# Performance work log

Hardware: AMD Instinct MI355X
Metric: run time of the kernel (lower is better)

Reference implementation:

```python
import jax, jax.numpy as jnp
import numpy as np
import math

B, S, E, H = 4, 2048, 1024, 16
D = E // H  # head_dim = 64
ROPE_BASE = 10000.0


def setup_inputs() -> dict:
    key = jax.random.key(0)
    ks = jax.random.split(key, 8)
    wscale = 1.0 / math.sqrt(E)
    inp = {
        "query": jax.random.normal(ks[0], (B, S, E), dtype=jnp.float32),
        "key": jax.random.normal(ks[1], (B, S, E), dtype=jnp.float32),
        "value": jax.random.normal(ks[2], (B, S, E), dtype=jnp.float32),
        "Wq": jax.random.normal(ks[3], (E, E), dtype=jnp.float32) * wscale,
        "Wk": jax.random.normal(ks[4], (E, E), dtype=jnp.float32) * wscale,
        "Wv": jax.random.normal(ks[5], (E, E), dtype=jnp.float32) * wscale,
        "Wo": jax.random.normal(ks[6], (E, E), dtype=jnp.float32) * wscale,
        "positions": jnp.arange(S, dtype=jnp.int64),
        # True = masked (upper triangle -> causal)
        "attn_mask": jnp.triu(jnp.ones((S, S), dtype=bool), k=1),
    }
    return inp


def _apply_rope(x, positions):
    # x: [B, H, S, D]; rotate-half RoPE convention
    half = D // 2
    inv_freq = 1.0 / (ROPE_BASE ** (jnp.arange(0, D, 2, dtype=jnp.float32) / D))  # [D/2]
    ang = positions.astype(jnp.float32)[:, None] * inv_freq[None, :]  # [S, D/2]
    cos = jnp.concatenate([jnp.cos(ang), jnp.cos(ang)], axis=-1)  # [S, D]
    sin = jnp.concatenate([jnp.sin(ang), jnp.sin(ang)], axis=-1)  # [S, D]
    x1, x2 = x[..., :half], x[..., half:]
    rot = jnp.concatenate([-x2, x1], axis=-1)
    return x * cos[None, None] + rot * sin[None, None]


def reference(query, key, value, Wq, Wk, Wv, Wo, positions, attn_mask):
    # projections (no bias, weight layout [out, in] as in set_weights_from_float)
    q = jnp.einsum('bse,oe->bso', query, Wq).reshape(B, S, H, D).transpose(0, 2, 1, 3)
    k = jnp.einsum('bse,oe->bso', key, Wk).reshape(B, S, H, D).transpose(0, 2, 1, 3)
    v = jnp.einsum('bse,oe->bso', value, Wv).reshape(B, S, H, D).transpose(0, 2, 1, 3)
    q = _apply_rope(q, positions)
    k = _apply_rope(k, positions)
    scale = 1.0 / math.sqrt(D)
    scores = jnp.einsum('bhqd,bhkd->bhqk', q, k) * scale  # [B,H,S,S]
    scores = jnp.where(attn_mask[None, None], -jnp.inf, scores)
    weights = jax.nn.softmax(scores, axis=-1)
    out = jnp.einsum('bhqk,bhkd->bhqd', weights, v)  # [B,H,S,D]
    out = out.transpose(0, 2, 1, 3).reshape(B, S, H * D)
    return jnp.einsum('bso,eo->bse', out, Wo)
```

## Files before the change

### kernel.cpp

```cpp
#include <hip/hip_runtime.h>
#include <hip/hip_bf16.h>
#include <math.h>

typedef __bf16 bf16;
typedef __attribute__((ext_vector_type(8))) __bf16 bf16x8;
typedef __attribute__((ext_vector_type(4))) __bf16 bf16x4;
typedef __attribute__((ext_vector_type(4))) float f32x4;
typedef __attribute__((ext_vector_type(16))) float f32x16;
typedef __attribute__((ext_vector_type(4))) unsigned uint4v;

#define MFMA16 __builtin_amdgcn_mfma_f32_16x16x32_bf16
#define MFMA32 __builtin_amdgcn_mfma_f32_32x32x16_bf16

__device__ __forceinline__ void g2l16(const void* g, void* l) {
    __builtin_amdgcn_global_load_lds(
        (const __attribute__((address_space(1))) void*)g,
        (__attribute__((address_space(3))) void*)l, 16, 0, 0);
}

__device__ __forceinline__ bool is_bf16_buf(const void* p) {
    const int lane = threadIdx.x & 63;
    unsigned w = ((const unsigned*)p)[lane];
    unsigned e = (w >> 7) & 0xFF;
    bool pl = (e == 0) || (e >= 80 && e < 134);
    return __popcll(__ballot(pl)) >= 52;
}

__device__ __forceinline__ void stage_f32(bf16* l, const float* g) {
    float4 f0 = ((const float4*)g)[0];
    float4 f1 = ((const float4*)g)[1];
    bf16x8 t;
    t[0] = (bf16)f0.x; t[1] = (bf16)f0.y; t[2] = (bf16)f0.z; t[3] = (bf16)f0.w;
    t[4] = (bf16)f1.x; t[5] = (bf16)f1.y; t[6] = (bf16)f1.z; t[7] = (bf16)f1.w;
    *(bf16x8*)l = t;
}

__device__ __forceinline__ unsigned cvtpk_bf16(float a, float b) {
    unsigned r;
    asm("v_cvt_pk_bf16_f32 %0, %1, %2" : "=v"(r) : "v"(a), "v"(b));
    return r;
}

__global__ __launch_bounds__(256) void convert7(const void* s0, const void* s1,
                                                const void* s2, const void* s3,
                                                const void* s4, const void* s5,
                                                const void* s6,
                                                bf16* __restrict__ dst) {
    const size_t e = ((size_t)blockIdx.x * 256 + threadIdx.x) * 8;
    const void* src; size_t off; bf16* d;
    if (e < 25165824) {
        const int i = (int)(e >> 23);
        src = i == 0 ? s0 : i == 1 ? s1 : s2;
        off = e & 8388607;
        d   = dst + ((size_t)i << 23) + off;
    } else {
        const size_t e2 = e - 25165824;
        const int i = (int)(e2 >> 20);
        src = i == 0 ? s3 : i == 1 ? s4 : i == 2 ? s5 : s6;
        off = e2 & 1048575;
        d   = dst + 25165824 + ((size_t)i << 20) + off;
    }
    if (is_bf16_buf(src)) {
        *(bf16x8*)d = *((const bf16x8*)((const bf16*)src + off));
    } else {
        stage_f32(d, (const float*)src + off);
    }
}

__device__ __forceinline__ void epi_rope(f32x4 acc[4][4], bf16* __restrict__ C,
                                         int m0, int n0, int wm, int wn,
                                         int quad, int l16, float scale) {
    const float kf = 0.41524101186092029f;
    const float inv0 = exp2f(-(float)l16 * kf);
    const float inv1 = exp2f(-(float)(l16 + 16) * kf);
#pragma unroll
    for (int mi = 0; mi < 4; mi++) {
#pragma unroll
        for (int r = 0; r < 4; r++) {
            const int row = m0 + wm + mi * 16 + quad * 4 + r;
            const float pos = (float)(row & 2047);
#pragma unroll
            for (int p = 0; p < 2; p++) {
                float sn, cs;
                __sincosf(pos * (p ? inv1 : inv0), &sn, &cs);
                const float x1 = acc[mi][p][r];
                const float x2 = acc[mi][p + 2][r];
                const int col = n0 + wn + p * 16 + l16;
                C[(size_t)row * 1024 + col]      = (bf16)((x1 * cs - x2 * sn) * scale);
                C[(size_t)row * 1024 + col + 32] = (bf16)((x2 * cs + x1 * sn) * scale);
            }
        }
    }
}

__device__ __forceinline__ void epi_vt(f32x4 acc[4][4], bf16* __restrict__ C,
                                       int m0, int n0, int wm, int wn,
                                       int quad, int l16) {
#pragma unroll
    for (int mi = 0; mi < 4; mi++) {
        const int rbase = m0 + wm + mi * 16 + quad * 4;
#pragma unroll
        for (int ni = 0; ni < 4; ni++) {
            const int col = n0 + wn + ni * 16 + l16;
            bf16x4 t;
#pragma unroll
            for (int r = 0; r < 4; r++) t[r] = (bf16)acc[mi][ni][r];
            *(bf16x4*)&C[(size_t)col * 8192 + rbase] = t;
        }
    }
}

__global__ __launch_bounds__(256) void gemm_qkv(const bf16* __restrict__ xq,
                                                const bf16* __restrict__ xk,
                                                const bf16* __restrict__ xv,
                                                const bf16* __restrict__ wq,
                                                const bf16* __restrict__ wk,
                                                const bf16* __restrict__ wv,
                                                bf16* __restrict__ Qp,
                                                bf16* __restrict__ Kp,
                                                bf16* __restrict__ Vt) {
    __shared__ bf16 As[128 * 32];
    __shared__ bf16 Bs[128 * 32];
    const int tid  = threadIdx.x;
    const int wave = tid >> 6;
    const int lane = tid & 63;
    const int quad = lane >> 4;
    const int l16  = lane & 15;
    const int z  = blockIdx.z;
    const int m0 = blockIdx.x * 128;
    const int n0 = blockIdx.y * 128;
    const int wm = (wave >> 1) * 64;
    const int wn = (wave & 1) * 64;

    const bf16* A = z == 0 ? xq : z == 1 ? xk : xv;
    const bf16* W = z == 0 ? wq : z == 1 ? wk : wv;

    const int ra = tid >> 2;
    const int c8 = (tid & 3) * 8;
    const bf16* ga = A + (size_t)(m0 + ra) * 1024 + c8;
    const bf16* gb = W + (size_t)(n0 + ra) * 1024 + c8;
    bf16* lA0 = As + (wave * 64) * 8;
    bf16* lA1 = As + (256 + wave * 64) * 8;
    bf16* lB0 = Bs + (wave * 64) * 8;
    bf16* lB1 = Bs + (256 + wave * 64) * 8;

    f32x4 acc[4][4] = {};

    for (int k0 = 0; k0 < 1024; k0 += 32) {
        __syncthreads();
        g2l16(ga + k0,             lA0);
        g2l16(ga + 64 * 1024 + k0, lA1);
        g2l16(gb + k0,             lB0);
        g2l16(gb + 64 * 1024 + k0, lB1);
        __syncthreads();

        bf16x8 af[4], bfb[4];
#pragma unroll
        for (int i = 0; i < 4; i++)
            af[i] = *(const bf16x8*)&As[(wm + i * 16 + l16) * 32 + quad * 8];
#pragma unroll
        for (int i = 0; i < 4; i++)
            bfb[i] = *(const bf16x8*)&Bs[(wn + i * 16 + l16) * 32 + quad * 8];
#pragma unroll
        for (int mi = 0; mi < 4; mi++)
#pragma unroll
            for (int ni = 0; ni < 4; ni++)
                acc[mi][ni] = MFMA16(af[mi], bfb[ni], acc[mi][ni], 0, 0, 0);
    }

    if (z == 0)      epi_rope(acc, Qp, m0, n0, wm, wn, quad, l16, 0.125f);
    else if (z == 1) epi_rope(acc, Kp, m0, n0, wm, wn, quad, l16, 1.0f);
    else             epi_vt  (acc, Vt, m0, n0, wm, wn, quad, l16);
}

__global__ __launch_bounds__(256) void gemm_nt(const void* __restrict__ Ap,
                                               const void* __restrict__ Wp,
                                               bf16* __restrict__ C,
                                               float* __restrict__ Cf,
                                               int mode, float scale) {
    __shared__ bf16 As[128 * 32];
    __shared__ bf16 Bs[128 * 32];
    const int tid  = threadIdx.x;
    const int wave = tid >> 6;
    const int lane = tid & 63;
    const int quad = lane >> 4;
    const int l16  = lane & 15;
    const int m0 = blockIdx.x * 128;
    const int n0 = blockIdx.y * 128;
    const int wm = (wave >> 1) * 64;
    const int wn = (wave & 1) * 64;

    const bool a_bf = is_bf16_buf(Ap);
    const bool b_bf = is_bf16_buf(Wp);

    const int ra = tid >> 2;
    const int c8 = (tid & 3) * 8;
    const bf16*  gaB = (const bf16*)Ap  + (size_t)(m0 + ra) * 1024 + c8;
    const bf16*  gbB = (const bf16*)Wp  + (size_t)(n0 + ra) * 1024 + c8;
    const float* gaF = (const float*)Ap + (size_t)(m0 + ra) * 1024 + c8;
    const float* gbF = (const float*)Wp + (size_t)(n0 + ra) * 1024 + c8;
    bf16* lA0 = As + (wave * 64) * 8;
    bf16* lA1 = As + (256 + wave * 64) * 8;
    bf16* lB0 = Bs + (wave * 64) * 8;
    bf16* lB1 = Bs + (256 + wave * 64) * 8;

    f32x4 acc[4][4] = {};

    for (int k0 = 0; k0 < 1024; k0 += 32) {
        __syncthreads();
        if (a_bf) {
            g2l16(gaB + k0,             lA0);
            g2l16(gaB + 64 * 1024 + k0, lA1);
        } else {
            stage_f32(As + tid * 8,        gaF + k0);
            stage_f32(As + 2048 + tid * 8, gaF + 64 * 1024 + k0);
        }
        if (b_bf) {
            g2l16(gbB + k0,             lB0);
            g2l16(gbB + 64 * 1024 + k0, lB1);
        } else {
            stage_f32(Bs + tid * 8,        gbF + k0);
            stage_f32(Bs + 2048 + tid * 8, gbF + 64 * 1024 + k0);
        }
        __syncthreads();

        bf16x8 af[4], bfb[4];
#pragma unroll
        for (int i = 0; i < 4; i++)
            af[i] = *(const bf16x8*)&As[(wm + i * 16 + l16) * 32 + quad * 8];
#pragma unroll
        for (int i = 0; i < 4; i++)
            bfb[i] = *(const bf16x8*)&Bs[(wn + i * 16 + l16) * 32 + quad * 8];
#pragma unroll
        for (int mi = 0; mi < 4; mi++)
#pragma unroll
            for (int ni = 0; ni < 4; ni++)
                acc[mi][ni] = MFMA16(af[mi], bfb[ni], acc[mi][ni], 0, 0, 0);
    }

    if (mode == 2) {
#pragma unroll
        for (int mi = 0; mi < 4; mi++) {
            const int rbase = m0 + wm + mi * 16 + quad * 4;
#pragma unroll
            for (int ni = 0; ni < 4; ni++) {
                const int col = n0 + wn + ni * 16 + l16;
#pragma unroll
                for (int r = 0; r < 4; r++)
                    Cf[(size_t)(rbase + r) * 1024 + col] = acc[mi][ni][r];
            }
        }
    } else if (mode == 3) {
        epi_vt(acc, C, m0, n0, wm, wn, quad, l16);
    } else if (mode == 0) {
#pragma unroll
        for (int mi = 0; mi < 4; mi++) {
            const int rbase = m0 + wm + mi * 16 + quad * 4;
#pragma unroll
            for (int ni = 0; ni < 4; ni++) {
                const int col = n0 + wn + ni * 16 + l16;
#pragma unroll
                for (int r = 0; r < 4; r++)
                    C[(size_t)(rbase + r) * 1024 + col] = (bf16)acc[mi][ni][r];
            }
        }
    } else {
        epi_rope(acc, C, m0, n0, wm, wn, quad, l16, scale);
    }
}

__global__ __launch_bounds__(512, 2) void attn_kernel(const bf16* __restrict__ Qp,
                                                      const bf16* __restrict__ Kp,
                                                      const bf16* __restrict__ Vt,
                                                      bf16* __restrict__ Op) {
    __shared__ bf16 Ks[2][64 * 64];
    __shared__ bf16 Vs[2][64 * 64];
    __shared__ bf16 Qs[256 * 64];
    const int tid  = threadIdx.x;
    const int wave = tid >> 6;
    const int lane = tid & 63;
    const int l31  = lane & 31;
    const int hi   = lane >> 5;
    const int bh = blockIdx.x;
    const int y  = blockIdx.y;
    const int qt = (y < 4) ? y : 11 - y;
    const int b  = bh >> 4;
    const int h  = bh & 15;
    const int q0 = qt * 256;
    const int jmax = 4 * qt + 3;
    const size_t baseqk = ((size_t)b * 2048) * 1024 + (size_t)h * 64;
    const bf16* Qg = Qp + baseqk;
    const bf16* Kg = Kp + baseqk;
    const bf16* Vg = Vt + (size_t)(h * 64) * 8192 + (size_t)b * 2048;
    bf16* Og = Op + baseqk;

    const int sr  = tid >> 3;
    const int swz = (((tid & 7) ^ (sr & 7)) * 8);

#pragma unroll
    for (int c = 0; c < 4; c++)
        g2l16(Qg + (size_t)(q0 + c * 64 + sr) * 1024 + swz, Qs + c * 4096 + wave * 512);
    g2l16(Kg + (size_t)sr * 1024 + swz, &Ks[0][wave * 512]);
    g2l16(Vg + (size_t)sr * 8192 + swz, &Vs[0][wave * 512]);
    __syncthreads();

    const int qr = wave * 32 + l31;
    bf16x8 qf[4];
#pragma unroll
    for (int t = 0; t < 4; t++)
        qf[t] = *(const bf16x8*)&Qs[qr * 64 + (((2 * t + hi) ^ (l31 & 7)) * 8)];

    bf16x8 ones;
#pragma unroll
    for (int i = 0; i < 8; i++) ones[i] = (bf16)1.0f;

    f32x16 o0 = {}, o1 = {}, lacc = {};

    for (int j = 0; j <= jmax; j++) {
        if (j) __syncthreads();
        if (j < jmax) {
            const int pb = (j + 1) & 1;
            g2l16(Kg + (size_t)((j + 1) * 64 + sr) * 1024 + swz, &Ks[pb][wave * 512]);
            g2l16(Vg + (size_t)sr * 8192 + (j + 1) * 64 + swz,   &Vs[pb][wave * 512]);
        }
        if (q0 + wave * 32 + 31 < j * 64) continue;
        const bf16* kb = Ks[j & 1];
        const bf16* vb = Vs[j & 1];

        f32x16 s0 = {}, s1 = {};
        __builtin_amdgcn_s_setprio(1);
#pragma unroll
        for (int t = 0; t < 4; t++) {
            const int g = ((2 * t + hi) ^ (l31 & 7)) * 8;
            bf16x8 kf0 = *(const bf16x8*)&kb[l31 * 64 + g];
            bf16x8 kf1 = *(const bf16x8*)&kb[(32 + l31) * 64 + g];
            s0 = MFMA32(kf0, qf[t], s0, 0, 0, 0);
            s1 = MFMA32(kf1, qf[t], s1, 0, 0, 0);
        }
        __builtin_amdgcn_s_setprio(0);

        if (j * 64 + 63 > q0 + wave * 32) {
            const int qg  = q0 + wave * 32 + l31;
            const int kb0 = j * 64 + 4 * hi;
#pragma unroll
            for (int r = 0; r < 16; r++) {
                const int krow = (r & 3) + 8 * (r >> 2);
                if (kb0 + krow > qg)      s0[r] = -INFINITY;
                if (kb0 + 32 + krow > qg) s1[r] = -INFINITY;
            }
        }

#pragma unroll
        for (int r = 0; r < 16; r++) {
            s0[r] = __expf(s0[r] - 12.0f);
            s1[r] = __expf(s1[r] - 12.0f);
        }

        __builtin_amdgcn_s_setprio(1);
#pragma unroll
        for (int ks = 0; ks < 4; ks++) {
            const f32x16 p = (ks < 2) ? s0 : s1;
            const int rb = 8 * (ks & 1);
            unsigned x0 = cvtpk_bf16(p[rb + 0], p[rb + 1]);
            unsigned x1 = cvtpk_bf16(p[rb + 2], p[rb + 3]);
            unsigned y0 = cvtpk_bf16(p[rb + 4], p[rb + 5]);
            unsigned y1 = cvtpk_bf16(p[rb + 6], p[rb + 7]);
            auto r0 = __builtin_amdgcn_permlane32_swap(x0, y0, false, false);
            auto r1 = __builtin_amdgcn_permlane32_swap(x1, y1, false, false);
            uint4v pw;
            pw.x = (unsigned)r0[0];
            pw.y = (unsigned)r1[0];
            pw.z = (unsigned)r0[1];
            pw.w = (unsigned)r1[1];
            const bf16x8 pa = __builtin_bit_cast(bf16x8, pw);

            lacc = MFMA32(pa, ones, lacc, 0, 0, 0);
            const int g = ((2 * ks + hi) ^ (l31 & 7)) * 8;
            bf16x8 vf0 = *(const bf16x8*)&vb[l31 * 64 + g];
            bf16x8 vf1 = *(const bf16x8*)&vb[(32 + l31) * 64 + g];
            o0 = MFMA32(pa, vf0, o0, 0, 0, 0);
            o1 = MFMA32(pa, vf1, o1, 0, 0, 0);
        }
        __builtin_amdgcn_s_setprio(0);
    }

#pragma unroll
    for (int r = 0; r < 16; r++) {
        const float linv = 1.0f / lacc[r];
        const int row = q0 + wave * 32 + (r & 3) + 8 * (r >> 2) + 4 * hi;
        Og[(size_t)row * 1024 + l31]      = (bf16)(o0[r] * linv);
        Og[(size_t)row * 1024 + 32 + l31] = (bf16)(o1[r] * linv);
    }
}

extern "C" void kernel_launch(void* const* d_in, const int* in_sizes, int n_in,
                              void* d_out, int out_size, void* d_ws, size_t ws_size,
                              hipStream_t stream) {
    const void* q  = d_in[0];
    const void* k  = d_in[1];
    const void* v  = d_in[2];
    const void* Wq = d_in[3];
    const void* Wk = d_in[4];
    const void* Wv = d_in[5];
    const void* Wo = d_in[6];
    float* out = (float*)d_out;

    const size_t M8 = (size_t)8192 * 1024;
    bf16* Qp  = (bf16*)d_ws;
    bf16* Kp  = Qp + M8;
    bf16* Vtp = Kp + M8;
    bf16* Ao  = Vtp + M8;
    bf16* cbase = Ao + M8;
    const size_t NEED = (M8 * 4 + 29360128) * sizeof(bf16);

    dim3 blk(256);
    dim3 gg(64, 8);

    if (ws_size >= NEED) {
        convert7<<<14336, blk, 0, stream>>>(q, k, v, Wq, Wk, Wv, Wo, cbase);
        const bf16* aq = cbase;
        const bf16* ak = cbase + M8;
        const bf16* av = cbase + 2 * M8;
        const bf16* wq = cbase + 3 * M8;
        const bf16* wk = wq + 1048576;
        const bf16* wv = wk + 1048576;
        const bf16* wo = wv + 1048576;
        gemm_qkv<<<dim3(64, 8, 3), blk, 0, stream>>>(aq, ak, av, wq, wk, wv,
                                                     Qp, Kp, Vtp);
        attn_kernel<<<dim3(64, 8), dim3(512), 0, stream>>>(Qp, Kp, Vtp, Ao);
        gemm_nt<<<gg, blk, 0, stream>>>(Ao, wo, nullptr, out, 2, 1.0f);
    } else {
        gemm_nt<<<gg, blk, 0, stream>>>(q, Wq, Qp, nullptr, 1, 0.125f);
        gemm_nt<<<gg, blk, 0, stream>>>(k, Wk, Kp, nullptr, 1, 1.0f);
        gemm_nt<<<gg, blk, 0, stream>>>(v, Wv, Vtp, nullptr, 3, 1.0f);
        attn_kernel<<<dim3(64, 8), dim3(512), 0, stream>>>(Qp, Kp, Vtp, Ao);
        gemm_nt<<<gg, blk, 0, stream>>>(Ao, Wo, nullptr, out, 2, 1.0f);
    }
}
```

Before: 307.5 us.

## Replace projection GEMMs with triple-buffered swizzled 128x256 MFMA core

Adds a shared GEMM core that uses 512-thread blocks with 128x256 tiles, a K-step of 64, and a three-stage LDS ring filled by direct global-to-LDS loads. Explicit vmcnt waits let loads for later tiles overlap with MFMA work, and an XOR swizzle on the LDS layout is meant to avoid bank conflicts. Both the QKV projection and the output projection use this core, replacing the old single-buffered 128x128 kernel that synchronised twice per 32-wide K step. The larger tiles halve the grid and use more LDS per block, which may lower occupancy.

```diff
diff --git a/kernel.cpp b/kernel.cpp
--- a/kernel.cpp
+++ b/kernel.cpp
@@ -110,67 +110,127 @@
     }
 }
 
-__global__ __launch_bounds__(256) void gemm_qkv(const bf16* __restrict__ xq,
-                                                const bf16* __restrict__ xk,
-                                                const bf16* __restrict__ xv,
-                                                const bf16* __restrict__ wq,
-                                                const bf16* __restrict__ wk,
-                                                const bf16* __restrict__ wv,
-                                                bf16* __restrict__ Qp,
-                                                bf16* __restrict__ Kp,
-                                                bf16* __restrict__ Vt) {
-    __shared__ bf16 As[128 * 32];
-    __shared__ bf16 Bs[128 * 32];
+__device__ __forceinline__ void gemm_core(const bf16* __restrict__ A,
+                                          const bf16* __restrict__ B,
+                                          int m0, int n0, f32x4 acc[4][4]) {
+    __shared__ bf16 As[3 * 8192];
+    __shared__ bf16 Bs[3 * 16384];
     const int tid  = threadIdx.x;
     const int wave = tid >> 6;
     const int lane = tid & 63;
     const int quad = lane >> 4;
     const int l16  = lane & 15;
+    const int wm   = (wave >> 2) * 64;
+    const int wn   = (wave & 3) * 64;
+    const int rowt = tid >> 3;
+    const int swz  = (((tid & 7) ^ (rowt & 7)) * 8);
+    const bf16* gA = A + (size_t)(m0 + rowt) * 1024 + swz;
+    const bf16* gB = B + (size_t)(n0 + rowt) * 1024 + swz;
+    bf16* AsW = As + wave * 512;
+    bf16* BsW = Bs + wave * 512;
+
+#define STAGE(t, b)                                                     \
+    do {                                                                \
+        const int k0_ = (t) * 64;                                       \
+        g2l16(gA + k0_,          AsW + (b) * 8192);                     \
+        g2l16(gA + 65536 + k0_,  AsW + (b) * 8192 + 4096);              \
+        g2l16(gB + k0_,          BsW + (b) * 16384);                    \
+        g2l16(gB + 65536 + k0_,  BsW + (b) * 16384 + 4096);             \
+        g2l16(gB + 131072 + k0_, BsW + (b) * 16384 + 8192);             \
+        g2l16(gB + 196608 + k0_, BsW + (b) * 16384 + 12288);            \
+    } while (0)
+
+    STAGE(0, 0);
+    STAGE(1, 1);
+
+    const int gsw0 = ((0 + quad) ^ (l16 & 7)) * 8;
+    const int gsw1 = ((4 + quad) ^ (l16 & 7)) * 8;
+
+#pragma unroll
+    for (int t = 0; t < 16; t++) {
+        if (t < 15) asm volatile("s_waitcnt vmcnt(6)" ::: "memory");
+        else        asm volatile("s_waitcnt vmcnt(0)" ::: "memory");
+        __builtin_amdgcn_s_barrier();
+        __builtin_amdgcn_sched_barrier(0);
+        if (t <= 13) STAGE(t + 2, (t + 2) % 3);
+        __builtin_amdgcn_sched_barrier(0);
+        const bf16* At = As + (t % 3) * 8192;
+        const bf16* Bt = Bs + (t % 3) * 16384;
+#pragma unroll
+        for (int kk = 0; kk < 2; kk++) {
+            const int gg = kk ? gsw1 : gsw0;
+            bf16x8 af[4], bfr[4];
+#pragma unroll
+            for (int i = 0; i < 4; i++)
+                af[i] = *(const bf16x8*)&At[(wm + i * 16 + l16) * 64 + gg];
+#pragma unroll
+            for (int i = 0; i < 4; i++)
+                bfr[i] = *(const bf16x8*)&Bt[(wn + i * 16 + l16) * 64 + gg];
+            __builtin_amdgcn_s_setprio(1);
+#pragma unroll
+            for (int mi = 0; mi < 4; mi++)
+#pragma unroll
+                for (int ni = 0; ni < 4; ni++)
+                    acc[mi][ni] = MFMA16(af[mi], bfr[ni], acc[mi][ni], 0, 0, 0);
+            __builtin_amdgcn_s_setprio(0);
+            __builtin_amdgcn_sched_barrier(0);
+            if (kk == 0) __builtin_amdgcn_s_barrier();
+        }
+    }
+#undef STAGE
+}
+
+__global__ __launch_bounds__(512) void qkv256(const bf16* __restrict__ xq,
+                                              const bf16* __restrict__ xk,
+                                              const bf16* __restrict__ xv,
+                                              const bf16* __restrict__ wq,
+                                              const bf16* __restrict__ wk,
+                                              const bf16* __restrict__ wv,
+                                              bf16* __restrict__ Qp,
+                                              bf16* __restrict__ Kp,
+                                              bf16* __restrict__ Vt) {
     const int z  = blockIdx.z;
     const int m0 = blockIdx.x * 128;
-    const int n0 = blockIdx.y * 128;
-    const int wm = (wave >> 1) * 64;
-    const int wn = (wave & 1) * 64;
-
+    const int n0 = blockIdx.y * 256;
     const bf16* A = z == 0 ? xq : z == 1 ? xk : xv;
     const bf16* W = z == 0 ? wq : z == 1 ? wk : wv;
-
-    const int ra = tid >> 2;
-    const int c8 = (tid & 3) * 8;
-    const bf16* ga = A + (size_t)(m0 + ra) * 1024 + c8;
-    const bf16* gb = W + (size_t)(n0 + ra) * 1024 + c8;
-    bf16* lA0 = As + (wave * 64) * 8;
-    bf16* lA1 = As + (256 + wave * 64) * 8;
-    bf16* lB0 = Bs + (wave * 64) * 8;
-    bf16* lB1 = Bs + (256 + wave * 64) * 8;
-
     f32x4 acc[4][4] = {};
-
-    for (int k0 = 0; k0 < 1024; k0 += 32) {
-        __syncthreads();
-        g2l16(ga + k0,             lA0);
-        g2l16(ga + 64 * 1024 + k0, lA1);
-        g2l16(gb + k0,             lB0);
-        g2l16(gb + 64 * 1024 + k0, lB1);
-        __syncthreads();
-
-        bf16x8 af[4], bfb[4];
-#pragma unroll
-        for (int i = 0; i < 4; i++)
-            af[i] = *(const bf16x8*)&As[(wm + i * 16 + l16) * 32 + quad * 8];
-#pragma unroll
-        for (int i = 0; i < 4; i++)
-            bfb[i] = *(const bf16x8*)&Bs[(wn + i * 16 + l16) * 32 + quad * 8];
-#pragma unroll
-        for (int mi = 0; mi < 4; mi++)
-#pragma unroll
-            for (int ni = 0; ni < 4; ni++)
-                acc[mi][ni] = MFMA16(af[mi], bfb[ni], acc[mi][ni], 0, 0, 0);
-    }
-
+    gemm_core(A, W, m0, n0, acc);
+    const int wave = threadIdx.x >> 6;
+    const int lane = threadIdx.x & 63;
+    const int quad = lane >> 4;
+    const int l16  = lane & 15;
+    const int wm = (wave >> 2) * 64;
+    const int wn = (wave & 3) * 64;
     if (z == 0)      epi_rope(acc, Qp, m0, n0, wm, wn, quad, l16, 0.125f);
     else if (z == 1) epi_rope(acc, Kp, m0, n0, wm, wn, quad, l16, 1.0f);
     else             epi_vt  (acc, Vt, m0, n0, wm, wn, quad, l16);
+}
+
+__global__ __launch_bounds__(512) void out256(const bf16* __restrict__ Ao,
+                                              const bf16* __restrict__ wo,
+                                              float* __restrict__ Cf) {
+    const int m0 = blockIdx.x * 128;
+    const int n0 = blockIdx.y * 256;
+    f32x4 acc[4][4] = {};
+    gemm_core(Ao, wo, m0, n0, acc);
+    const int wave = threadIdx.x >> 6;
+    const int lane = threadIdx.x & 63;
+    const int quad = lane >> 4;
+    const int l16  = lane & 15;
+    const int wm = (wave >> 2) * 64;
+    const int wn = (wave & 3) * 64;
+#pragma unroll
+    for (int mi = 0; mi < 4; mi++) {
+        const int rbase = m0 + wm + mi * 16 + quad * 4;
+#pragma unroll
+        for (int ni = 0; ni < 4; ni++) {
+            const int col = n0 + wn + ni * 16 + l16;
+#pragma unroll
+            for (int r = 0; r < 4; r++)
+                Cf[(size_t)(rbase + r) * 1024 + col] = acc[mi][ni][r];
+        }
+    }
 }
 
 __global__ __launch_bounds__(256) void gemm_nt(const void* __restrict__ Ap,
@@ -425,10 +485,10 @@
         const bf16* wk = wq + 1048576;
         const bf16* wv = wk + 1048576;
         const bf16* wo = wv + 1048576;
-        gemm_qkv<<<dim3(64, 8, 3), blk, 0, stream>>>(aq, ak, av, wq, wk, wv,
-                                                     Qp, Kp, Vtp);
+        qkv256<<<dim3(64, 4, 3), dim3(512), 0, stream>>>(aq, ak, av, wq, wk, wv,
+                                                         Qp, Kp, Vtp);
         attn_kernel<<<dim3(64, 8), dim3(512), 0, stream>>>(Qp, Kp, Vtp, Ao);
-        gemm_nt<<<gg, blk, 0, stream>>>(Ao, wo, nullptr, out, 2, 1.0f);
+        out256<<<dim3(64, 4), dim3(512), 0, stream>>>(Ao, wo, out);
     } else {
         gemm_nt<<<gg, blk, 0, stream>>>(q, Wq, Qp, nullptr, 1, 0.125f);
         gemm_nt<<<gg, blk, 0, stream>>>(k, Wk, Kp, nullptr, 1, 1.0f);
```

After: 299.2 us. -2.7%, faster.
